# Performance work log

Measured on AMD Instinct MI355X. Metric: run time of the kernel, lower is better.

Reference implementation:

```python
import jax, jax.numpy as jnp
import numpy as np

H = 2048
L = 3  # conv_L_cache


def setup_inputs() -> dict:
    key = jax.random.key(0)
    k1, k2, k3, k4 = jax.random.split(key, 4)
    hidden_states = jax.random.normal(k1, (2, 4096, H), dtype=jnp.float32)
    W_in = jax.random.normal(k2, (3 * H, H), dtype=jnp.float32) * 0.02
    conv_w = jax.random.normal(k3, (H, 1, L), dtype=jnp.float32) * 0.1
    W_out = jax.random.normal(k4, (H, H), dtype=jnp.float32) * 0.02
    return {"hidden_states": hidden_states, "W_in": W_in, "conv_w": conv_w, "W_out": W_out}


def reference(hidden_states, W_in, conv_w, W_out):
    # in_proj: [b, s, H] @ [H, 3H] -> [b, s, 3H]
    BCx = jnp.einsum('bsh,gh->bsg', hidden_states, W_in)
    B, C, x = jnp.split(BCx, 3, axis=-1)  # each [b, s, H]
    Bx = (B * x).transpose(0, 2, 1)       # [b, H, s] pre-conv gating
    # depthwise causal conv1d, kernel L, left pad L-1 (== Conv1d pad L-1 then [:seqlen])
    conv_out = jax.lax.conv_general_dilated(
        Bx, conv_w,
        window_strides=(1,),
        padding=[(L - 1, 0)],
        feature_group_count=H,
        dimension_numbers=('NCH', 'OIH', 'NCH'),
    )  # [b, H, s]
    y = C.transpose(0, 2, 1) * conv_out   # post-conv gating, [b, H, s]
    y = y.transpose(0, 2, 1)              # [b, s, H]
    return jnp.einsum('bsh,oh->bso', y, W_out)
```

## Files before the change

kernel.cpp:

```cpp
#include <hip/hip_runtime.h>
#include <hip/hip_bf16.h>
#include <stdint.h>

typedef __bf16 bf16;
typedef __bf16 bf16x8 __attribute__((ext_vector_type(8)));
typedef float floatx16 __attribute__((ext_vector_type(16)));

__global__ __launch_bounds__(256) void cast_f32_bf16(
    const float* __restrict__ in, bf16* __restrict__ out, int n)
{
    int i = (blockIdx.x * 256 + threadIdx.x) * 8;
    if (i >= n) return;
    float4 a = *(const float4*)(in + i);
    float4 b = *(const float4*)(in + i + 4);
    bf16x8 o;
    o[0] = (bf16)a.x; o[1] = (bf16)a.y; o[2] = (bf16)a.z; o[3] = (bf16)a.w;
    o[4] = (bf16)b.x; o[5] = (bf16)b.y; o[6] = (bf16)b.z; o[7] = (bf16)b.w;
    *(bf16x8*)(out + i) = o;
}

__device__ __forceinline__ void load_lds16(const bf16* g, bf16* l) {
    __builtin_amdgcn_global_load_lds(
        (const __attribute__((address_space(1))) void*)g,
        (__attribute__((address_space(3))) void*)l, 16, 0, 0);
}

#define VMCNT(N) asm volatile("s_waitcnt vmcnt(" #N ")" ::: "memory")

template <typename CT>
__global__ __launch_bounds__(512, 2) void gemm_bt(
    const bf16* __restrict__ A, const bf16* __restrict__ Bt, CT* __restrict__ C,
    int M, int N, int K)
{
    __shared__ __align__(16) bf16 As[4 * 8192];
    __shared__ __align__(16) bf16 Bs[4 * 8192];

    const int tid = threadIdx.x;
    const int w     = tid >> 6;
    const int l     = tid & 63;
    const int wm    = w & 1;
    const int wn    = w >> 1;
    const int lm32  = l & 31;
    const int lhalf = l >> 5;

    const int mBase = blockIdx.y * 256;
    const int nBase = blockIdx.x * 256;

    const int rowT  = tid >> 2;
    const int lchnk = (tid & 3) ^ ((((tid >> 3) & 1) << 1) | ((tid >> 4) & 1));
    const int kelm  = lchnk * 8;

    const bf16* gA0 = A  + (size_t)(mBase + rowT) * K + kelm;
    const bf16* gA1 = gA0 + (size_t)128 * K;
    const bf16* gB0 = Bt + (size_t)(nBase + rowT) * K + kelm;
    const bf16* gB1 = gB0 + (size_t)128 * K;

    bf16* lA = As + tid * 8;
    bf16* lB = Bs + tid * 8;

    const int swz = (((lm32 >> 1) & 1) << 1) | ((lm32 >> 2) & 1);
    const int fA0 = (wm * 128 + lm32) * 32 + ((0 + lhalf) ^ swz) * 8;
    const int fA1 = (wm * 128 + lm32) * 32 + ((2 + lhalf) ^ swz) * 8;
    const int fB0 = (wn * 64  + lm32) * 32 + ((0 + lhalf) ^ swz) * 8;
    const int fB1 = (wn * 64  + lm32) * 32 + ((2 + lhalf) ^ swz) * 8;

#define STAGE(kt) do {                                   \
        const int _b = ((kt) & 3) * 8192;                \
        const int _o = (kt) * 32;                        \
        load_lds16(gA0 + _o, lA + _b);                   \
        load_lds16(gA1 + _o, lA + _b + 4096);            \
        load_lds16(gB0 + _o, lB + _b);                   \
        load_lds16(gB1 + _o, lB + _b + 4096);            \
    } while (0)

#define KSTEP(tt, NCNT) do {                                              \
        VMCNT(NCNT);                                                      \
        __builtin_amdgcn_s_barrier();                                     \
        asm volatile("" ::: "memory");                                    \
        __builtin_amdgcn_sched_barrier(0);                                \
        const bf16* Ab = As + ((tt) & 3) * 8192;                          \
        const bf16* Bb = Bs + ((tt) & 3) * 8192;                          \
        bf16x8 a0[4], a1[4], b0[2], b1[2];                                \
        _Pragma("unroll")                                                 \
        for (int i = 0; i < 4; ++i) {                                     \
            a0[i] = *(const bf16x8*)(Ab + fA0 + i * 1024);                \
            a1[i] = *(const bf16x8*)(Ab + fA1 + i * 1024);                \
        }                                                                 \
        _Pragma("unroll")                                                 \
        for (int j = 0; j < 2; ++j) {                                     \
            b0[j] = *(const bf16x8*)(Bb + fB0 + j * 1024);                \
            b1[j] = *(const bf16x8*)(Bb + fB1 + j * 1024);                \
        }                                                                 \
        __builtin_amdgcn_s_setprio(1);                                    \
        _Pragma("unroll")                                                 \
        for (int i = 0; i < 4; ++i)                                       \
            _Pragma("unroll")                                             \
            for (int j = 0; j < 2; ++j) {                                 \
                acc[i][j] = __builtin_amdgcn_mfma_f32_32x32x16_bf16(      \
                    a0[i], b0[j], acc[i][j], 0, 0, 0);                    \
                acc[i][j] = __builtin_amdgcn_mfma_f32_32x32x16_bf16(      \
                    a1[i], b1[j], acc[i][j], 0, 0, 0);                    \
            }                                                             \
        __builtin_amdgcn_s_setprio(0);                                    \
        __builtin_amdgcn_sched_barrier(0);                                \
        asm volatile("s_waitcnt lgkmcnt(0)" ::: "memory");                \
        __builtin_amdgcn_sched_barrier(0);                                \
        __builtin_amdgcn_s_barrier();                                     \
        asm volatile("" ::: "memory");                                    \
    } while (0)

    floatx16 acc[4][2] = {};

    STAGE(0); STAGE(1); STAGE(2);

    const int kIters = K / 32;
    int kt = 0;
    for (; kt < kIters - 3; ++kt) {
        STAGE(kt + 3);
        KSTEP(kt, 12);
    }
    KSTEP(kt, 8); ++kt;
    KSTEP(kt, 4); ++kt;
    KSTEP(kt, 0);

#undef STAGE
#undef KSTEP

    #pragma unroll
    for (int i = 0; i < 4; ++i) {
        #pragma unroll
        for (int j = 0; j < 2; ++j) {
            const int col = nBase + wn * 64 + j * 32 + lm32;
            const int rB  = mBase + wm * 128 + i * 32 + 4 * lhalf;
            #pragma unroll
            for (int r = 0; r < 16; ++r) {
                const int row = rB + (r & 3) + 8 * (r >> 2);
                C[(size_t)row * N + col] = (CT)acc[i][j][r];
            }
        }
    }
}

__global__ __launch_bounds__(256) void conv_gate(
    const bf16* __restrict__ BCx, const float* __restrict__ convw,
    bf16* __restrict__ Y)
{
    const int tx = threadIdx.x;
    const int h0 = tx * 8;
    const int bb = blockIdx.y;
    const int s0 = blockIdx.x * 32;

    float w0[8], w1[8], w2[8];
    #pragma unroll
    for (int j = 0; j < 8; ++j) {
        w0[j] = convw[(h0 + j) * 3 + 0];
        w1[j] = convw[(h0 + j) * 3 + 1];
        w2[j] = convw[(h0 + j) * 3 + 2];
    }

    const size_t mB = (size_t)bb * 4096;

    float bx1[8], bx2[8];
    #pragma unroll
    for (int j = 0; j < 8; ++j) { bx1[j] = 0.f; bx2[j] = 0.f; }
    if (s0 >= 2) {
        const bf16* r1 = BCx + (mB + s0 - 1) * 6144;
        const bf16* r2 = BCx + (mB + s0 - 2) * 6144;
        bf16x8 B1 = *(const bf16x8*)(r1 + h0);
        bf16x8 x1 = *(const bf16x8*)(r1 + 4096 + h0);
        bf16x8 B2 = *(const bf16x8*)(r2 + h0);
        bf16x8 x2 = *(const bf16x8*)(r2 + 4096 + h0);
        #pragma unroll
        for (int j = 0; j < 8; ++j) {
            bx1[j] = (float)B1[j] * (float)x1[j];
            bx2[j] = (float)B2[j] * (float)x2[j];
        }
    }

    for (int s = s0; s < s0 + 32; ++s) {
        const size_t m = mB + s;
        const bf16* rp = BCx + m * 6144;
        bf16x8 Bv = *(const bf16x8*)(rp + h0);
        bf16x8 Cv = *(const bf16x8*)(rp + 2048 + h0);
        bf16x8 xv = *(const bf16x8*)(rp + 4096 + h0);
        bf16x8 o;
        #pragma unroll
        for (int j = 0; j < 8; ++j) {
            float bx0 = (float)Bv[j] * (float)xv[j];
            float cv  = w0[j] * bx2[j] + w1[j] * bx1[j] + w2[j] * bx0;
            o[j] = (bf16)((float)Cv[j] * cv);
            bx2[j] = bx1[j];
            bx1[j] = bx0;
        }
        *(bf16x8*)(Y + m * 2048 + h0) = o;
    }
}

extern "C" void kernel_launch(void* const* d_in, const int* in_sizes, int n_in,
                              void* d_out, int out_size, void* d_ws, size_t ws_size,
                              hipStream_t stream) {
    const float* hidden = (const float*)d_in[0];
    const float* Win    = (const float*)d_in[1];
    const float* convw  = (const float*)d_in[2];
    const float* Wout   = (const float*)d_in[3];
    float* out = (float*)d_out;

    const int nH = 8192 * 2048;
    const int nWin = 6144 * 2048;
    const int nWout = 2048 * 2048;

    bf16* hB    = (bf16*)d_ws;
    bf16* WinB  = hB + (size_t)nH;
    bf16* WoutB = WinB + (size_t)nWin;
    bf16* BCx   = WoutB + (size_t)nWout;
    bf16* Y     = BCx + (size_t)8192 * 6144;

    cast_f32_bf16<<<nH / (256 * 8), 256, 0, stream>>>(hidden, hB, nH);
    cast_f32_bf16<<<nWin / (256 * 8), 256, 0, stream>>>(Win, WinB, nWin);
    cast_f32_bf16<<<nWout / (256 * 8), 256, 0, stream>>>(Wout, WoutB, nWout);

    gemm_bt<bf16><<<dim3(6144 / 256, 8192 / 256), dim3(512), 0, stream>>>(
        hB, WinB, BCx, 8192, 6144, 2048);
    conv_gate<<<dim3(4096 / 32, 2), dim3(256), 0, stream>>>(BCx, convw, Y);
    gemm_bt<float><<<dim3(2048 / 256, 8192 / 256), dim3(512), 0, stream>>>(
        Y, WoutB, out, 8192, 2048, 2048);
}
```

Baseline: 517.8 us.

## Rewrite GEMM mainloop as 8-phase ping-pong schedule with 16x16x32 MFMA

Restructures the bf16 GEMM inner loop from a 4-stage ring of 32-wide K tiles into a double-buffered 64-wide K tile scheme. Loads are split into half-tiles interleaved with register-fragment reads and quarter-block MFMA groups across eight phases per iteration. It also switches from 32x32x16 to 16x16x32 MFMA with a new LDS swizzle and output mapping. The goal is finer-grained overlap of global->LDS loads, LDS reads and MFMA, but it adds more barriers per K step and relies on subtle vmcnt accounting. Wrapped-around prefetches at the tail issue redundant loads.

```diff
diff --git a/kernel.cpp b/kernel.cpp
--- a/kernel.cpp
+++ b/kernel.cpp
@@ -4,7 +4,7 @@
 
 typedef __bf16 bf16;
 typedef __bf16 bf16x8 __attribute__((ext_vector_type(8)));
-typedef float floatx16 __attribute__((ext_vector_type(16)));
+typedef float floatx4 __attribute__((ext_vector_type(4)));
 
 __global__ __launch_bounds__(256) void cast_f32_bf16(
     const float* __restrict__ in, bf16* __restrict__ out, int n)
@@ -25,118 +25,147 @@
         (__attribute__((address_space(3))) void*)l, 16, 0, 0);
 }
 
-#define VMCNT(N) asm volatile("s_waitcnt vmcnt(" #N ")" ::: "memory")
+#define VMCNT(N)  asm volatile("s_waitcnt vmcnt(" #N ")" ::: "memory")
+#define LGKM0     do { asm volatile("s_waitcnt lgkmcnt(0)" ::: "memory"); \
+                       __builtin_amdgcn_sched_barrier(0); } while (0)
+#define BARRIER   do { asm volatile("" ::: "memory");                     \
+                       __builtin_amdgcn_s_barrier();                      \
+                       asm volatile("" ::: "memory"); } while (0)
 
 template <typename CT>
 __global__ __launch_bounds__(512, 2) void gemm_bt(
     const bf16* __restrict__ A, const bf16* __restrict__ Bt, CT* __restrict__ C,
     int M, int N, int K)
 {
-    __shared__ __align__(16) bf16 As[4 * 8192];
-    __shared__ __align__(16) bf16 Bs[4 * 8192];
+    __shared__ __align__(16) bf16 As[2 * 16384];
+    __shared__ __align__(16) bf16 Bs[2 * 16384];
 
     const int tid = threadIdx.x;
-    const int w     = tid >> 6;
-    const int l     = tid & 63;
-    const int wm    = w & 1;
-    const int wn    = w >> 1;
-    const int lm32  = l & 31;
-    const int lhalf = l >> 5;
+    const int l   = tid & 63;
+    const int w   = tid >> 6;
+    const int wm  = w & 1;
+    const int wn  = w >> 1;
+    const int rl  = l & 15;
+    const int kq  = l >> 4;
+    const int ck  = (kq ^ (((rl >> 2) & 1) << 1)) * 8;
 
     const int mBase = blockIdx.y * 256;
     const int nBase = blockIdx.x * 256;
 
-    const int rowT  = tid >> 2;
-    const int lchnk = (tid & 3) ^ ((((tid >> 3) & 1) << 1) | ((tid >> 4) & 1));
-    const int kelm  = lchnk * 8;
-
-    const bf16* gA0 = A  + (size_t)(mBase + rowT) * K + kelm;
-    const bf16* gA1 = gA0 + (size_t)128 * K;
-    const bf16* gB0 = Bt + (size_t)(nBase + rowT) * K + kelm;
-    const bf16* gB1 = gB0 + (size_t)128 * K;
-
-    bf16* lA = As + tid * 8;
-    bf16* lB = Bs + tid * 8;
-
-    const int swz = (((lm32 >> 1) & 1) << 1) | ((lm32 >> 2) & 1);
-    const int fA0 = (wm * 128 + lm32) * 32 + ((0 + lhalf) ^ swz) * 8;
-    const int fA1 = (wm * 128 + lm32) * 32 + ((2 + lhalf) ^ swz) * 8;
-    const int fB0 = (wn * 64  + lm32) * 32 + ((0 + lhalf) ^ swz) * 8;
-    const int fB1 = (wn * 64  + lm32) * 32 + ((2 + lhalf) ^ swz) * 8;
-
-#define STAGE(kt) do {                                   \
-        const int _b = ((kt) & 3) * 8192;                \
-        const int _o = (kt) * 32;                        \
-        load_lds16(gA0 + _o, lA + _b);                   \
-        load_lds16(gA1 + _o, lA + _b + 4096);            \
-        load_lds16(gB0 + _o, lB + _b);                   \
-        load_lds16(gB1 + _o, lB + _b + 4096);            \
-    } while (0)
-
-#define KSTEP(tt, NCNT) do {                                              \
-        VMCNT(NCNT);                                                      \
-        __builtin_amdgcn_s_barrier();                                     \
-        asm volatile("" ::: "memory");                                    \
-        __builtin_amdgcn_sched_barrier(0);                                \
-        const bf16* Ab = As + ((tt) & 3) * 8192;                          \
-        const bf16* Bb = Bs + ((tt) & 3) * 8192;                          \
-        bf16x8 a0[4], a1[4], b0[2], b1[2];                                \
+    const int aRd = wm * 8192 + rl * 64 + ck;
+    const int bRd = (wn >> 1) * 8192 + ((wn & 1) * 64 + rl) * 64 + ck;
+
+    const int srow = tid >> 3;
+    const int schk = (tid & 7) ^ (((tid >> 5) & 1) << 1);
+    const bf16* gA = A  + (size_t)(mBase + srow) * K + schk * 8;
+    const bf16* gB = Bt + (size_t)(nBase + srow) * K + schk * 8;
+    bf16* dA = As + tid * 8;
+    bf16* dB = Bs + tid * 8;
+    const size_t rowK64 = (size_t)64 * K;
+
+#define STAGE_A(T, h, buf) do {                                           \
+        const bf16* _g = gA + (size_t)(h) * 128 * K + (T) * 64;           \
+        bf16* _d = dA + (buf) * 16384 + (h) * 8192;                       \
+        load_lds16(_g, _d);                                               \
+        load_lds16(_g + rowK64, _d + 4096);                               \
+    } while (0)
+#define STAGE_B(T, h, buf) do {                                           \
+        const bf16* _g = gB + (size_t)(h) * 128 * K + (T) * 64;           \
+        bf16* _d = dB + (buf) * 16384 + (h) * 8192;                       \
+        load_lds16(_g, _d);                                               \
+        load_lds16(_g + rowK64, _d + 4096);                               \
+    } while (0)
+
+#define READ_A(dst, msub, buf) do {                                       \
         _Pragma("unroll")                                                 \
-        for (int i = 0; i < 4; ++i) {                                     \
-            a0[i] = *(const bf16x8*)(Ab + fA0 + i * 1024);                \
-            a1[i] = *(const bf16x8*)(Ab + fA1 + i * 1024);                \
+        for (int _i = 0; _i < 4; ++_i) {                                  \
+            _Pragma("unroll")                                             \
+            for (int _ks = 0; _ks < 2; ++_ks)                             \
+                dst[_i][_ks] = *(const bf16x8*)(As + (buf) * 16384 + aRd  \
+                    + (msub) * 4096 + _i * 1024 + _ks * 32);              \
         }                                                                 \
+    } while (0)
+#define READ_B(dst, nsub, buf) do {                                       \
         _Pragma("unroll")                                                 \
-        for (int j = 0; j < 2; ++j) {                                     \
-            b0[j] = *(const bf16x8*)(Bb + fB0 + j * 1024);                \
-            b1[j] = *(const bf16x8*)(Bb + fB1 + j * 1024);                \
+        for (int _j = 0; _j < 2; ++_j) {                                  \
+            _Pragma("unroll")                                             \
+            for (int _ks = 0; _ks < 2; ++_ks)                             \
+                dst[_j][_ks] = *(const bf16x8*)(Bs + (buf) * 16384 + bRd  \
+                    + (nsub) * 2048 + _j * 1024 + _ks * 32);              \
         }                                                                 \
+    } while (0)
+
+#define MFMA_Q(am, bn, MS, NS) do {                                       \
         __builtin_amdgcn_s_setprio(1);                                    \
         _Pragma("unroll")                                                 \
-        for (int i = 0; i < 4; ++i)                                       \
+        for (int _ks = 0; _ks < 2; ++_ks)                                 \
             _Pragma("unroll")                                             \
-            for (int j = 0; j < 2; ++j) {                                 \
-                acc[i][j] = __builtin_amdgcn_mfma_f32_32x32x16_bf16(      \
-                    a0[i], b0[j], acc[i][j], 0, 0, 0);                    \
-                acc[i][j] = __builtin_amdgcn_mfma_f32_32x32x16_bf16(      \
-                    a1[i], b1[j], acc[i][j], 0, 0, 0);                    \
-            }                                                             \
+            for (int _i = 0; _i < 4; ++_i)                                \
+                _Pragma("unroll")                                         \
+                for (int _j = 0; _j < 2; ++_j)                            \
+                    acc[(MS)*4 + _i][(NS)*2 + _j] =                       \
+                        __builtin_amdgcn_mfma_f32_16x16x32_bf16(          \
+                            am[_i][_ks], bn[_j][_ks],                     \
+                            acc[(MS)*4 + _i][(NS)*2 + _j], 0, 0, 0);      \
         __builtin_amdgcn_s_setprio(0);                                    \
-        __builtin_amdgcn_sched_barrier(0);                                \
-        asm volatile("s_waitcnt lgkmcnt(0)" ::: "memory");                \
-        __builtin_amdgcn_sched_barrier(0);                                \
-        __builtin_amdgcn_s_barrier();                                     \
-        asm volatile("" ::: "memory");                                    \
-    } while (0)
-
-    floatx16 acc[4][2] = {};
-
-    STAGE(0); STAGE(1); STAGE(2);
-
-    const int kIters = K / 32;
-    int kt = 0;
-    for (; kt < kIters - 3; ++kt) {
-        STAGE(kt + 3);
-        KSTEP(kt, 12);
-    }
-    KSTEP(kt, 8); ++kt;
-    KSTEP(kt, 4); ++kt;
-    KSTEP(kt, 0);
-
-#undef STAGE
-#undef KSTEP
+    } while (0)
+
+    floatx4 acc[8][4] = {};
+    bf16x8 a0[4][2], a1[4][2], b0[2][2], b1[2][2];
+
+    const int kIters = K >> 7;
+    const int nT     = K >> 6;
+
+    STAGE_B(0, 0, 0);
+    STAGE_A(0, 0, 0);
+    STAGE_A(0, 1, 0);
+    STAGE_B(0, 1, 0);
+    STAGE_B(1, 0, 1);
+    STAGE_A(1, 0, 1);
+    STAGE_A(1, 1, 1);
+    VMCNT(2);
+    BARRIER;
+    READ_A(a0, 0, 0);
+    READ_B(b0, 0, 0);
+
+    for (int it = 0; it < kIters; ++it) {
+        const int To  = 2 * it + 1;
+        int Te2 = 2 * it + 2; if (Te2 >= nT) Te2 -= nT;
+        int To2 = 2 * it + 3; if (To2 >= nT) To2 -= nT;
+
+        VMCNT(2); READ_B(b1, 1, 0); STAGE_B(To, 1, 1);
+        BARRIER; LGKM0; MFMA_Q(a0, b0, 0, 0);
+        VMCNT(2); READ_A(a1, 1, 0); STAGE_B(Te2, 0, 0);
+        BARRIER; LGKM0; MFMA_Q(a0, b1, 0, 1);
+        VMCNT(2); READ_A(a0, 0, 1); STAGE_A(Te2, 0, 0);
+        BARRIER; LGKM0; MFMA_Q(a1, b1, 1, 1);
+        VMCNT(2); READ_B(b1, 1, 1); STAGE_A(Te2, 1, 0);
+        BARRIER; LGKM0; MFMA_Q(a1, b0, 1, 0);
+        VMCNT(2); READ_B(b0, 0, 1); STAGE_B(Te2, 1, 0);
+        BARRIER; LGKM0; MFMA_Q(a0, b1, 0, 1);
+        VMCNT(2); READ_A(a1, 1, 1); STAGE_B(To2, 0, 1);
+        BARRIER; LGKM0; MFMA_Q(a0, b0, 0, 0);
+        VMCNT(2); READ_A(a0, 0, 0); STAGE_A(To2, 0, 1);
+        BARRIER; LGKM0; MFMA_Q(a1, b0, 1, 0);
+        VMCNT(2); READ_B(b0, 0, 0); STAGE_A(To2, 1, 1);
+        BARRIER; LGKM0; MFMA_Q(a1, b1, 1, 1);
+    }
+
+#undef STAGE_A
+#undef STAGE_B
+#undef READ_A
+#undef READ_B
+#undef MFMA_Q
 
     #pragma unroll
-    for (int i = 0; i < 4; ++i) {
+    for (int fi = 0; fi < 8; ++fi) {
         #pragma unroll
-        for (int j = 0; j < 2; ++j) {
-            const int col = nBase + wn * 64 + j * 32 + lm32;
-            const int rB  = mBase + wm * 128 + i * 32 + 4 * lhalf;
+        for (int fj = 0; fj < 4; ++fj) {
+            const int col = nBase + wn * 64 + fj * 16 + rl;
+            const int rB  = mBase + wm * 128 + fi * 16 + kq * 4;
             #pragma unroll
-            for (int r = 0; r < 16; ++r) {
-                const int row = rB + (r & 3) + 8 * (r >> 2);
-                C[(size_t)row * N + col] = (CT)acc[i][j][r];
-            }
+            for (int r = 0; r < 4; ++r)
+                C[(size_t)(rB + r) * N + col] = (CT)acc[fi][fj][r];
         }
     }
 }
```

Result: faster. 444.4 us (-14.2%).
